# Performance work log

Measured on AMD Instinct MI355X. Metric: run time of the kernel, lower is better.

The kernel has to match this reference:

```python
import jax, jax.numpy as jnp
import numpy as np

D_MODEL = 1024
N_HEADS = 16
D_HEAD = D_MODEL // N_HEADS
D_FF = 4096
THETA = 10000.0
EPS = 1e-5


def rmsnorm(x, g):
    xf = x.astype(jnp.float32)
    rms = jnp.sqrt(jnp.mean(xf * xf, axis=-1, keepdims=True) + EPS)
    return ((xf / rms) * g).astype(x.dtype)


def rope(x, pos):
    # x: (B, H, S, d_head); pos: (S,) int
    dk = x.shape[-1]
    inv_freq = 1.0 / (THETA ** (jnp.arange(0, dk, 2, dtype=jnp.float32) / dk))
    freqs = pos.astype(jnp.float32)[:, None] * inv_freq[None, :]  # (S, dk/2)
    cos, sin = jnp.cos(freqs), jnp.sin(freqs)
    xp = x.reshape(*x.shape[:-1], dk // 2, 2)
    xe, xo = xp[..., 0], xp[..., 1]
    re = xe * cos - xo * sin
    ro = xe * sin + xo * cos
    return jnp.stack([re, ro], axis=-1).reshape(x.shape)


def attention(x, pos, q_w, k_w, v_w, o_w):
    B, S, D = x.shape
    def heads(t):
        return t.reshape(B, S, N_HEADS, D_HEAD).transpose(0, 2, 1, 3)
    Q = heads(x @ q_w.T)
    K = heads(x @ k_w.T)
    V = heads(x @ v_w.T)
    Q = rope(Q, pos)
    K = rope(K, pos)
    scores = jnp.einsum('bhqd,bhkd->bhqk', Q, K) / jnp.sqrt(jnp.float32(D_HEAD))
    causal = jnp.tril(jnp.ones((S, S), dtype=bool))
    scores = jnp.where(causal[None, None], scores, -jnp.inf)
    attn = jax.nn.softmax(scores, axis=-1)
    H = jnp.einsum('bhqk,bhkd->bhqd', attn, V)
    H = H.transpose(0, 2, 1, 3).reshape(B, S, D)
    return H @ o_w.T


def swiglu(x, w1, w2, w3):
    a = x @ w1.T
    swish = a * jax.nn.sigmoid(a)
    gate = x @ w3.T
    return (swish * gate) @ w2.T


def setup_inputs() -> dict:
    key = jax.random.key(0)
    ks = jax.random.split(key, 8)
    B, S = 4, 2048
    std_ff = (2.0 / (D_MODEL + D_FF)) ** 0.5
    return {
        'x': jax.random.normal(ks[0], (B, S, D_MODEL), jnp.float32),
        'token_positions': jnp.arange(S, dtype=jnp.int32),
        'q_w': jax.random.truncated_normal(ks[1], -3, 3, (D_MODEL, D_MODEL), jnp.float32),
        'k_w': jax.random.truncated_normal(ks[2], -3, 3, (D_MODEL, D_MODEL), jnp.float32),
        'v_w': jax.random.truncated_normal(ks[3], -3, 3, (D_MODEL, D_MODEL), jnp.float32),
        'o_w': jax.random.truncated_normal(ks[4], -3, 3, (D_MODEL, D_MODEL), jnp.float32),
        'g1': jnp.ones((D_MODEL,), jnp.float32),
        'g2': jnp.ones((D_MODEL,), jnp.float32),
        'w1': jax.random.truncated_normal(ks[5], -3, 3, (D_FF, D_MODEL), jnp.float32) * std_ff,
        'w2': jax.random.truncated_normal(ks[6], -3, 3, (D_MODEL, D_FF), jnp.float32) * std_ff,
        'w3': jax.random.truncated_normal(ks[7], -3, 3, (D_FF, D_MODEL), jnp.float32) * std_ff,
    }


def reference(x, token_positions, q_w, k_w, v_w, o_w, g1, g2, w1, w2, w3):
    x_norm = rmsnorm(x, g1)
    O = x + attention(x_norm, token_positions, q_w, k_w, v_w, o_w)
    H = O + swiglu(rmsnorm(O, g2), w1, w2, w3)
    return H
```

## Files before the change

### kernel.cpp

```cpp
#include <hip/hip_runtime.h>
#include <stdint.h>


typedef short bf16x8 __attribute__((ext_vector_type(8)));
typedef float f32x4  __attribute__((ext_vector_type(4)));

#define DEV static __device__ __forceinline__

DEV float bf2f(uint32_t u) { uint32_t v = u << 16; float f; __builtin_memcpy(&f, &v, 4); return f; }
DEV uint16_t f2bf(float f) {
  uint32_t u; __builtin_memcpy(&u, &f, 4);
  u = (u + 0x7fffu + ((u >> 16) & 1u)) >> 16;
  return (uint16_t)u;
}

DEV void gl_lds16(const uint16_t* g, uint16_t* l) {
  __builtin_amdgcn_global_load_lds((const __attribute__((address_space(1))) uint32_t*)g,
                                   (__attribute__((address_space(3))) uint32_t*)l, 16, 0, 0);
}


__global__ __launch_bounds__(256) void cvt_bf16_k(const float* __restrict__ src,
                                                  uint16_t* __restrict__ dst, int n4) {
  const int t = blockIdx.x * 256 + threadIdx.x;
  if (t >= n4) return;
  const float4 v = ((const float4*)src)[t];
  ushort4 o; o.x = f2bf(v.x); o.y = f2bf(v.y); o.z = f2bf(v.z); o.w = f2bf(v.w);
  ((ushort4*)dst)[t] = o;
}

__global__ __launch_bounds__(256) void cvt_split_qk_k(const float* __restrict__ qw,
                                                      const float* __restrict__ kw,
                                                      uint16_t* __restrict__ hi,
                                                      uint16_t* __restrict__ lo) {
  const int t = blockIdx.x * 256 + threadIdx.x;
  const int row = t >> 8, c4 = t & 255;
  const float* src = (row < 1024) ? (qw + (size_t)row * 1024)
                                  : (kw + (size_t)(row - 1024) * 1024);
  const float4 v = ((const float4*)src)[c4];
  ushort4 h, l;
  h.x = f2bf(v.x); l.x = f2bf(v.x - bf2f(h.x));
  h.y = f2bf(v.y); l.y = f2bf(v.y - bf2f(h.y));
  h.z = f2bf(v.z); l.z = f2bf(v.z - bf2f(h.z));
  h.w = f2bf(v.w); l.w = f2bf(v.w - bf2f(h.w));
  ((ushort4*)hi)[t] = h; ((ushort4*)lo)[t] = l;
}


template <bool SPLIT>
__global__ __launch_bounds__(256) void rmsnorm_k(const float* __restrict__ xin,
                                                 const float* __restrict__ g,
                                                 uint16_t* __restrict__ hi,
                                                 uint16_t* __restrict__ lo) {
  const int row = blockIdx.x, t = threadIdx.x;
  const float4 v = ((const float4*)(xin + (size_t)row * 1024))[t];
  float ss = v.x * v.x + v.y * v.y + v.z * v.z + v.w * v.w;
#pragma unroll
  for (int m = 1; m < 64; m <<= 1) ss += __shfl_xor(ss, m);
  __shared__ float red[4];
  if ((t & 63) == 0) red[t >> 6] = ss;
  __syncthreads();
  const float rinv = rsqrtf((red[0] + red[1] + red[2] + red[3]) * (1.0f / 1024.0f) + 1e-5f);
  const float4 gv = ((const float4*)g)[t];
  float y[4] = { v.x * rinv * gv.x, v.y * rinv * gv.y, v.z * rinv * gv.z, v.w * rinv * gv.w };
  ushort4 h; h.x = f2bf(y[0]); h.y = f2bf(y[1]); h.z = f2bf(y[2]); h.w = f2bf(y[3]);
  ((ushort4*)(hi + (size_t)row * 1024))[t] = h;
  if constexpr (SPLIT) {
    ushort4 l;
    l.x = f2bf(y[0] - bf2f(h.x)); l.y = f2bf(y[1] - bf2f(h.y));
    l.z = f2bf(y[2] - bf2f(h.z)); l.w = f2bf(y[3] - bf2f(h.w));
    ((ushort4*)(lo + (size_t)row * 1024))[t] = l;
  }
}


template <int OUT>
__global__ __launch_bounds__(256) void gemm_bt_k(const uint16_t* __restrict__ A,
                                                 const uint16_t* __restrict__ B,
                                                 void* __restrict__ C,
                                                 const float* __restrict__ resid,
                                                 int N, int K) {
  __shared__ __align__(16) uint16_t As[128 * 64];
  __shared__ __align__(16) uint16_t Bs[128 * 64];
  const int t = threadIdx.x, w = t >> 6, lane = t & 63, m16 = lane & 15, quad = lane >> 4;
  const int wm = (w >> 1) * 64, wn = (w & 1) * 64;
  const int mBase = blockIdx.y * 128, nBase = blockIdx.x * 128;
  f32x4 acc[4][4];
  const f32x4 vz = {0.f, 0.f, 0.f, 0.f};
#pragma unroll
  for (int i = 0; i < 4; ++i)
#pragma unroll
    for (int j = 0; j < 4; ++j) acc[i][j] = vz;
  const int r_ = t >> 3, g_ = t & 7, sg = g_ ^ (r_ & 7);
  const uint16_t* ag = A + (size_t)(mBase + r_) * K + sg * 8;
  const uint16_t* bg = B + (size_t)(nBase + r_) * K + sg * 8;
  for (int k0 = 0; k0 < K; k0 += 64) {
#pragma unroll
    for (int it = 0; it < 4; ++it) {
      gl_lds16(ag + (size_t)(it * 32) * K + k0, As + it * 2048 + t * 8);
      gl_lds16(bg + (size_t)(it * 32) * K + k0, Bs + it * 2048 + t * 8);
    }
    __syncthreads();
#pragma unroll
    for (int ks = 0; ks < 2; ++ks) {
      bf16x8 af[4], bf4[4];
      const int cg = ks * 4 + quad;
#pragma unroll
      for (int i = 0; i < 4; ++i) {
        const int rA = wm + i * 16 + m16;
        af[i] = *(const bf16x8*)(As + rA * 64 + ((cg ^ (rA & 7)) * 8));
        const int rB = wn + i * 16 + m16;
        bf4[i] = *(const bf16x8*)(Bs + rB * 64 + ((cg ^ (rB & 7)) * 8));
      }
#pragma unroll
      for (int i = 0; i < 4; ++i)
#pragma unroll
        for (int j = 0; j < 4; ++j)
          acc[i][j] = __builtin_amdgcn_mfma_f32_16x16x32_bf16(af[i], bf4[j], acc[i][j], 0, 0, 0);
    }
    __syncthreads();
  }
#pragma unroll
  for (int i = 0; i < 4; ++i) {
    const int row0 = mBase + wm + i * 16 + quad * 4;
#pragma unroll
    for (int j = 0; j < 4; ++j) {
      const int col = nBase + wn + j * 16 + m16;
#pragma unroll
      for (int r = 0; r < 4; ++r) {
        const size_t idx = (size_t)(row0 + r) * N + col;
        const float v = acc[i][j][r];
        if constexpr (OUT == 1) ((float*)C)[idx] = v + resid[idx];
        else                    ((uint16_t*)C)[idx] = f2bf(v);
      }
    }
  }
}


template <int OUT>
__global__ __launch_bounds__(512, 2) void gemm256_k(const uint16_t* __restrict__ A,
                                                    const uint16_t* __restrict__ B,
                                                    uint16_t* __restrict__ C,
                                                    const uint16_t* __restrict__ aux,
                                                    int N, int K) {
  __shared__ __align__(16) uint16_t As[2][256 * 64];
  __shared__ __align__(16) uint16_t Bs[2][256 * 64];
  const int t = threadIdx.x, w = t >> 6, lane = t & 63, m16 = lane & 15, quad = lane >> 4;
  const int wm = (w >> 2) * 128, wn = (w & 3) * 64;
  const int mBase = blockIdx.y * 256, nBase = blockIdx.x * 256;
  const int NT = K >> 6;

  f32x4 acc[8][4];
  const f32x4 vz = {0.f, 0.f, 0.f, 0.f};
#pragma unroll
  for (int i = 0; i < 8; ++i)
#pragma unroll
    for (int j = 0; j < 4; ++j) acc[i][j] = vz;

  const int r_ = t >> 3, g_ = t & 7, sg = g_ ^ (r_ & 7);
  const uint16_t* ag = A + (size_t)(mBase + r_) * K + sg * 8;
  const uint16_t* bg = B + (size_t)(nBase + r_) * K + sg * 8;

#define STG_A(kt, h)                                                         \
  if ((kt) < NT) {                                                           \
    uint16_t* d0 = &As[(kt) & 1][(h) * 8192 + t * 8];                        \
    const uint16_t* s0 = ag + (size_t)((h) * 128) * K + (kt) * 64;           \
    gl_lds16(s0, d0);                                                        \
    gl_lds16(s0 + (size_t)64 * K, d0 + 4096);                                \
  }
#define STG_B(kt, h)                                                         \
  if ((kt) < NT) {                                                           \
    uint16_t* d0 = &Bs[(kt) & 1][(h) * 8192 + t * 8];                        \
    const uint16_t* s0 = bg + (size_t)((h) * 128) * K + (kt) * 64;           \
    gl_lds16(s0, d0);                                                        \
    gl_lds16(s0 + (size_t)64 * K, d0 + 4096);                                \
  }

  STG_B(0, 0); STG_B(0, 1); STG_A(0, 0); STG_A(0, 1);
  STG_B(1, 0); STG_A(1, 0);

  for (int T = 0; T < NT; ++T) {
    const int c = T & 1;
    const uint16_t* Ac = As[c];
    const uint16_t* Bc = Bs[c];
    bf16x8 af[4][2], b0[2][2], b1[2][2];

    STG_B(T + 1, 1);
    if (T == NT - 1) { asm volatile("s_waitcnt vmcnt(0)" ::: "memory"); }
    else             { asm volatile("s_waitcnt vmcnt(6)" ::: "memory"); }
    __builtin_amdgcn_s_barrier();
    __builtin_amdgcn_sched_barrier(0);
#pragma unroll
    for (int i = 0; i < 4; ++i) {
      const int rA = wm + i * 16 + m16;
#pragma unroll
      for (int ks = 0; ks < 2; ++ks)
        af[i][ks] = *(const bf16x8*)(Ac + rA * 64 + (((ks * 4 + quad) ^ (rA & 7)) * 8));
    }
#pragma unroll
    for (int j = 0; j < 2; ++j) {
      const int rB = wn + j * 16 + m16;
#pragma unroll
      for (int ks = 0; ks < 2; ++ks)
        b0[j][ks] = *(const bf16x8*)(Bc + rB * 64 + (((ks * 4 + quad) ^ (rB & 7)) * 8));
    }
    __builtin_amdgcn_s_setprio(1);
#pragma unroll
    for (int ks = 0; ks < 2; ++ks)
#pragma unroll
      for (int i = 0; i < 4; ++i)
#pragma unroll
        for (int j = 0; j < 2; ++j)
          acc[i][j] = __builtin_amdgcn_mfma_f32_16x16x32_bf16(af[i][ks], b0[j][ks], acc[i][j], 0, 0, 0);
    __builtin_amdgcn_s_setprio(0);
    __builtin_amdgcn_s_barrier();

    STG_A(T + 1, 1);
#pragma unroll
    for (int j = 0; j < 2; ++j) {
      const int rB = wn + (2 + j) * 16 + m16;
#pragma unroll
      for (int ks = 0; ks < 2; ++ks)
        b1[j][ks] = *(const bf16x8*)(Bc + rB * 64 + (((ks * 4 + quad) ^ (rB & 7)) * 8));
    }
    __builtin_amdgcn_s_setprio(1);
#pragma unroll
    for (int ks = 0; ks < 2; ++ks)
#pragma unroll
      for (int i = 0; i < 4; ++i)
#pragma unroll
        for (int j = 0; j < 2; ++j)
          acc[i][2 + j] = __builtin_amdgcn_mfma_f32_16x16x32_bf16(af[i][ks], b1[j][ks], acc[i][2 + j], 0, 0, 0);
    __builtin_amdgcn_s_setprio(0);
    __builtin_amdgcn_s_barrier();

    STG_B(T + 2, 0);
#pragma unroll
    for (int i = 0; i < 4; ++i) {
      const int rA = wm + 64 + i * 16 + m16;
#pragma unroll
      for (int ks = 0; ks < 2; ++ks)
        af[i][ks] = *(const bf16x8*)(Ac + rA * 64 + (((ks * 4 + quad) ^ (rA & 7)) * 8));
    }
    __builtin_amdgcn_s_setprio(1);
#pragma unroll
    for (int ks = 0; ks < 2; ++ks)
#pragma unroll
      for (int i = 0; i < 4; ++i)
#pragma unroll
        for (int j = 0; j < 2; ++j)
          acc[4 + i][j] = __builtin_amdgcn_mfma_f32_16x16x32_bf16(af[i][ks], b0[j][ks], acc[4 + i][j], 0, 0, 0);
    __builtin_amdgcn_s_setprio(0);
    __builtin_amdgcn_s_barrier();

    STG_A(T + 2, 0);
    __builtin_amdgcn_s_setprio(1);
#pragma unroll
    for (int ks = 0; ks < 2; ++ks)
#pragma unroll
      for (int i = 0; i < 4; ++i)
#pragma unroll
        for (int j = 0; j < 2; ++j)
          acc[4 + i][2 + j] = __builtin_amdgcn_mfma_f32_16x16x32_bf16(af[i][ks], b1[j][ks], acc[4 + i][2 + j], 0, 0, 0);
    __builtin_amdgcn_s_setprio(0);
    __builtin_amdgcn_s_barrier();
  }
#undef STG_A
#undef STG_B

#pragma unroll
  for (int i = 0; i < 8; ++i) {
    const int row0 = mBase + wm + i * 16 + quad * 4;
#pragma unroll
    for (int j = 0; j < 4; ++j) {
      const int col = nBase + wn + j * 16 + m16;
#pragma unroll
      for (int r = 0; r < 4; ++r) {
        const size_t idx = (size_t)(row0 + r) * N + col;
        const float v = acc[i][j][r];
        if constexpr (OUT == 2) {
          const float a = bf2f(aux[idx]);
          const float sw = a / (1.f + __expf(-a));
          C[idx] = f2bf(sw * v);
        } else {
          C[idx] = f2bf(v);
        }
      }
    }
  }
}


__global__ __launch_bounds__(512, 2) void gemm_split256_k(
    const uint16_t* __restrict__ Ahi, const uint16_t* __restrict__ Alo,
    const uint16_t* __restrict__ Bhi, const uint16_t* __restrict__ Blo,
    uint16_t* __restrict__ Chi, uint16_t* __restrict__ Clo, int N, int K) {
  __shared__ __align__(16) uint16_t Ah[2][256 * 32];
  __shared__ __align__(16) uint16_t Al[2][256 * 32];
  __shared__ __align__(16) uint16_t Bh[2][256 * 32];
  __shared__ __align__(16) uint16_t Bl[2][256 * 32];
  const int t = threadIdx.x, w = t >> 6, lane = t & 63, m16 = lane & 15, quad = lane >> 4;
  const int wm = (w >> 2) * 128, wn = (w & 3) * 64;
  const int mBase = blockIdx.y * 256, nBase = blockIdx.x * 256;
  const int NT = K >> 5;

  f32x4 acc[8][4];
  const f32x4 vz = {0.f, 0.f, 0.f, 0.f};
#pragma unroll
  for (int i = 0; i < 8; ++i)
#pragma unroll
    for (int j = 0; j < 4; ++j) acc[i][j] = vz;

  const int r_ = t >> 2, g_ = t & 3, sg = g_ ^ (r_ & 3);
  const uint16_t* agh = Ahi + (size_t)(mBase + r_) * K + sg * 8;
  const uint16_t* agl = Alo + (size_t)(mBase + r_) * K + sg * 8;
  const uint16_t* bgh = Bhi + (size_t)(nBase + r_) * K + sg * 8;
  const uint16_t* bgl = Blo + (size_t)(nBase + r_) * K + sg * 8;

#define STG4(OP, base, kt)                                                   \
  if ((kt) < NT) {                                                           \
    uint16_t* d = &OP[(kt) & 1][t * 8];                                      \
    const uint16_t* s = (base) + (size_t)(kt) * 32;                          \
    gl_lds16(s, d);                                                          \
    gl_lds16(s + (size_t)128 * K, d + 4096);                                 \
  }

  STG4(Bh, bgh, 0); STG4(Bl, bgl, 0);
  STG4(Ah, agh, 0); STG4(Al, agl, 0);
  STG4(Bh, bgh, 1); STG4(Bl, bgl, 1);

  for (int T = 0; T < NT; ++T) {
    const int c = T & 1;
    bf16x8 a_h[4], a_l[4], b0h[2], b0l[2], b1h[2], b1l[2];

    STG4(Ah, agh, T + 1);
    if (T == NT - 1) { asm volatile("s_waitcnt vmcnt(0)" ::: "memory"); }
    else             { asm volatile("s_waitcnt vmcnt(6)" ::: "memory"); }
    __builtin_amdgcn_s_barrier();
    __builtin_amdgcn_sched_barrier(0);
#pragma unroll
    for (int i = 0; i < 4; ++i) {
      const int rA = wm + i * 16 + m16;
      const int offA = rA * 32 + ((quad ^ (rA & 3)) * 8);
      a_h[i] = *(const bf16x8*)(&Ah[c][offA]);
      a_l[i] = *(const bf16x8*)(&Al[c][offA]);
    }
#pragma unroll
    for (int j = 0; j < 2; ++j) {
      const int rB = wn + j * 16 + m16;
      const int offB = rB * 32 + ((quad ^ (rB & 3)) * 8);
      b0h[j] = *(const bf16x8*)(&Bh[c][offB]);
      b0l[j] = *(const bf16x8*)(&Bl[c][offB]);
    }
    __builtin_amdgcn_s_setprio(1);
#pragma unroll
    for (int i = 0; i < 4; ++i)
#pragma unroll
      for (int j = 0; j < 2; ++j) {
        acc[i][j] = __builtin_amdgcn_mfma_f32_16x16x32_bf16(a_h[i], b0h[j], acc[i][j], 0, 0, 0);
        acc[i][j] = __builtin_amdgcn_mfma_f32_16x16x32_bf16(a_h[i], b0l[j], acc[i][j], 0, 0, 0);
        acc[i][j] = __builtin_amdgcn_mfma_f32_16x16x32_bf16(a_l[i], b0h[j], acc[i][j], 0, 0, 0);
      }
    __builtin_amdgcn_s_setprio(0);
    __builtin_amdgcn_s_barrier();

    STG4(Al, agl, T + 1);
#pragma unroll
    for (int j = 0; j < 2; ++j) {
      const int rB = wn + (2 + j) * 16 + m16;
      const int offB = rB * 32 + ((quad ^ (rB & 3)) * 8);
      b1h[j] = *(const bf16x8*)(&Bh[c][offB]);
      b1l[j] = *(const bf16x8*)(&Bl[c][offB]);
    }
    __builtin_amdgcn_s_setprio(1);
#pragma unroll
    for (int i = 0; i < 4; ++i)
#pragma unroll
      for (int j = 0; j < 2; ++j) {
        acc[i][2 + j] = __builtin_amdgcn_mfma_f32_16x16x32_bf16(a_h[i], b1h[j], acc[i][2 + j], 0, 0, 0);
        acc[i][2 + j] = __builtin_amdgcn_mfma_f32_16x16x32_bf16(a_h[i], b1l[j], acc[i][2 + j], 0, 0, 0);
        acc[i][2 + j] = __builtin_amdgcn_mfma_f32_16x16x32_bf16(a_l[i], b1h[j], acc[i][2 + j], 0, 0, 0);
      }
    __builtin_amdgcn_s_setprio(0);
    __builtin_amdgcn_s_barrier();

    STG4(Bh, bgh, T + 2);
#pragma unroll
    for (int i = 0; i < 4; ++i) {
      const int rA = wm + 64 + i * 16 + m16;
      const int offA = rA * 32 + ((quad ^ (rA & 3)) * 8);
      a_h[i] = *(const bf16x8*)(&Ah[c][offA]);
      a_l[i] = *(const bf16x8*)(&Al[c][offA]);
    }
    __builtin_amdgcn_s_setprio(1);
#pragma unroll
    for (int i = 0; i < 4; ++i)
#pragma unroll
      for (int j = 0; j < 2; ++j) {
        acc[4 + i][j] = __builtin_amdgcn_mfma_f32_16x16x32_bf16(a_h[i], b0h[j], acc[4 + i][j], 0, 0, 0);
        acc[4 + i][j] = __builtin_amdgcn_mfma_f32_16x16x32_bf16(a_h[i], b0l[j], acc[4 + i][j], 0, 0, 0);
        acc[4 + i][j] = __builtin_amdgcn_mfma_f32_16x16x32_bf16(a_l[i], b0h[j], acc[4 + i][j], 0, 0, 0);
      }
    __builtin_amdgcn_s_setprio(0);
    __builtin_amdgcn_s_barrier();

    STG4(Bl, bgl, T + 2);
    __builtin_amdgcn_s_setprio(1);
#pragma unroll
    for (int i = 0; i < 4; ++i)
#pragma unroll
      for (int j = 0; j < 2; ++j) {
        acc[4 + i][2 + j] = __builtin_amdgcn_mfma_f32_16x16x32_bf16(a_h[i], b1h[j], acc[4 + i][2 + j], 0, 0, 0);
        acc[4 + i][2 + j] = __builtin_amdgcn_mfma_f32_16x16x32_bf16(a_h[i], b1l[j], acc[4 + i][2 + j], 0, 0, 0);
        acc[4 + i][2 + j] = __builtin_amdgcn_mfma_f32_16x16x32_bf16(a_l[i], b1h[j], acc[4 + i][2 + j], 0, 0, 0);
      }
    __builtin_amdgcn_s_setprio(0);
    __builtin_amdgcn_s_barrier();
  }
#undef STG4

#pragma unroll
  for (int i = 0; i < 8; ++i) {
    const int row0 = mBase + wm + i * 16 + quad * 4;
#pragma unroll
    for (int j = 0; j < 4; ++j) {
      const int col = nBase + wn + j * 16 + m16;
#pragma unroll
      for (int r = 0; r < 4; ++r) {
        const size_t idx = (size_t)(row0 + r) * N + col;
        const float v = acc[i][j][r];
        const uint16_t hh = f2bf(v);
        Chi[idx] = hh;
        Clo[idx] = f2bf(v - bf2f(hh));
      }
    }
  }
}


__global__ __launch_bounds__(256) void rope_k(uint16_t* __restrict__ qkh,
                                              uint16_t* __restrict__ qkl,
                                              const int* __restrict__ pos) {
  const int u = blockIdx.x * 256 + threadIdx.x;
  const int row = u >> 8, p = (u & 255) * 4;
  const int which = p >> 9, hp = p & 511, h = hp >> 5, d2 = hp & 31;
  const size_t idx = (size_t)row * 2048 + which * 1024 + h * 64 + d2 * 2;
  union { uint4 v; uint32_t w[4]; } vh, vl, oh, ol;
  vh.v = *(const uint4*)(qkh + idx);
  vl.v = *(const uint4*)(qkl + idx);
  const float fp = (float)pos[row & 2047];
#pragma unroll
  for (int e = 0; e < 4; ++e) {
    const float xe = bf2f(vh.w[e] & 0xffffu) + bf2f(vl.w[e] & 0xffffu);
    const float xo = bf2f(vh.w[e] >> 16) + bf2f(vl.w[e] >> 16);
    const float inv_freq = exp2f((float)(d2 + e) * -0.41524101186092029f);
    const float fr = fp * inv_freq;
    float sn, cs; sincosf(fr, &sn, &cs);
    const float re = xe * cs - xo * sn;
    const float ro = xe * sn + xo * cs;
    const uint16_t reh = f2bf(re), roh = f2bf(ro);
    const uint16_t rel = f2bf(re - bf2f(reh)), rol = f2bf(ro - bf2f(roh));
    oh.w[e] = (uint32_t)reh | ((uint32_t)roh << 16);
    ol.w[e] = (uint32_t)rel | ((uint32_t)rol << 16);
  }
  *(uint4*)(qkh + idx) = oh.v;
  *(uint4*)(qkl + idx) = ol.v;
}


__global__ __launch_bounds__(256) void flash_k(const uint16_t* __restrict__ Qh,
                                               const uint16_t* __restrict__ Ql,
                                               const uint16_t* __restrict__ Vt,
                                               uint16_t* __restrict__ Hout) {
  __shared__ __align__(16) uint16_t Kh[2][64 * 64];
  __shared__ __align__(16) uint16_t Kl[2][64 * 64];
  __shared__ __align__(16) uint16_t Vs[2][64 * 64];
  __shared__ __align__(16) uint16_t P[4][32 * 72];

  const int bh = blockIdx.y, b = bh >> 4, h = bh & 15;
  const int t = threadIdx.x, w = t >> 6, lane = t & 63, m16 = lane & 15, quad = lane >> 4;

  const int r_ = t >> 3, g_ = t & 7, sgx = g_ ^ (r_ & 7);
  const uint16_t* khg = Qh + (size_t)(b * 2048 + r_) * 2048 + 1024 + h * 64 + sgx * 8;
  const uint16_t* klg = Ql + (size_t)(b * 2048 + r_) * 2048 + 1024 + h * 64 + sgx * 8;
  const uint16_t* vtg = Vt + (size_t)(h * 64 + r_) * 8192 + (size_t)b * 2048 + sgx * 8;

  const float nscl = 0.18033688011112042f;

  for (int half = 0; half < 2; ++half) {
    const int qt = half ? (15 - (int)blockIdx.x) : (int)blockIdx.x;

    bf16x8 qh[2][2], ql[2][2];
#pragma unroll
    for (int i = 0; i < 2; ++i) {
      const int row = b * 2048 + qt * 128 + w * 32 + i * 16 + m16;
#pragma unroll
      for (int ks = 0; ks < 2; ++ks) {
        const size_t offq = (size_t)row * 2048 + h * 64 + ks * 32 + quad * 8;
        qh[i][ks] = *(const bf16x8*)(Qh + offq);
        ql[i][ks] = *(const bf16x8*)(Ql + offq);
      }
    }
#pragma unroll
    for (int i = 0; i < 2; ++i)
#pragma unroll
      for (int ks = 0; ks < 2; ++ks)
        asm volatile("" : "+v"(qh[i][ks]), "+v"(ql[i][ks]));

    const int ktEnd = 2 * qt + 2;

#pragma unroll
    for (int it = 0; it < 2; ++it) {
      gl_lds16(khg + (size_t)(it * 32) * 2048, &Kh[0][it * 2048 + t * 8]);
      gl_lds16(klg + (size_t)(it * 32) * 2048, &Kl[0][it * 2048 + t * 8]);
      gl_lds16(vtg + (size_t)(it * 32) * 8192, &Vs[0][it * 2048 + t * 8]);
    }

    float mr[2][4], lr[2][4];
    f32x4 o[2][4];
    const f32x4 vz = {0.f, 0.f, 0.f, 0.f};
#pragma unroll
    for (int i = 0; i < 2; ++i)
#pragma unroll
      for (int r = 0; r < 4; ++r) { mr[i][r] = -1e30f; lr[i][r] = 0.f; }
#pragma unroll
    for (int i = 0; i < 2; ++i)
#pragma unroll
      for (int n = 0; n < 4; ++n) o[i][n] = vz;

    for (int kt = 0; kt < ktEnd; ++kt) {
      const int cur = kt & 1, nxt = cur ^ 1;
      __builtin_amdgcn_s_barrier();
      __builtin_amdgcn_sched_barrier(0);
      if (kt + 1 < ktEnd) {
        const int kn = kt + 1;
#pragma unroll
        for (int it = 0; it < 2; ++it) {
          gl_lds16(khg + (size_t)(kn * 64 + it * 32) * 2048, &Kh[nxt][it * 2048 + t * 8]);
          gl_lds16(klg + (size_t)(kn * 64 + it * 32) * 2048, &Kl[nxt][it * 2048 + t * 8]);
          gl_lds16(vtg + (size_t)(it * 32) * 8192 + kn * 64, &Vs[nxt][it * 2048 + t * 8]);
        }
        asm volatile("s_waitcnt vmcnt(6)" ::: "memory");
      } else {
        asm volatile("s_waitcnt vmcnt(0)" ::: "memory");
      }
      __builtin_amdgcn_s_barrier();
      __builtin_amdgcn_sched_barrier(0);

      f32x4 sc[2][4];
#pragma unroll
      for (int i = 0; i < 2; ++i)
#pragma unroll
        for (int j = 0; j < 4; ++j) sc[i][j] = vz;
#pragma unroll
      for (int ks = 0; ks < 2; ++ks) {
        bf16x8 kfh[4], kfl[4];
        const int cg = ks * 4 + quad;
#pragma unroll
        for (int j = 0; j < 4; ++j) {
          const int rK = j * 16 + m16;
          const int offk = rK * 64 + ((cg ^ (rK & 7)) * 8);
          kfh[j] = *(const bf16x8*)(&Kh[cur][offk]);
          kfl[j] = *(const bf16x8*)(&Kl[cur][offk]);
        }
        __builtin_amdgcn_s_setprio(1);
#pragma unroll
        for (int i = 0; i < 2; ++i)
#pragma unroll
          for (int j = 0; j < 4; ++j) {
            sc[i][j] = __builtin_amdgcn_mfma_f32_16x16x32_bf16(qh[i][ks], kfh[j], sc[i][j], 0, 0, 0);
            sc[i][j] = __builtin_amdgcn_mfma_f32_16x16x32_bf16(qh[i][ks], kfl[j], sc[i][j], 0, 0, 0);
            sc[i][j] = __builtin_amdgcn_mfma_f32_16x16x32_bf16(ql[i][ks], kfh[j], sc[i][j], 0, 0, 0);
          }
        __builtin_amdgcn_s_setprio(0);
      }

#pragma unroll
      for (int i = 0; i < 2; ++i) {
        const bool needMask = (kt * 64 + 63) > (qt * 128 + w * 32 + i * 16);
#pragma unroll
        for (int r = 0; r < 4; ++r) {
          float mx = -1e30f;
          if (needMask) {
            const int qg = qt * 128 + w * 32 + i * 16 + quad * 4 + r;
#pragma unroll
            for (int j = 0; j < 4; ++j) {
              float v = sc[i][j][r];
              const int kg = kt * 64 + j * 16 + m16;
              if (kg > qg) v = -1e30f;
              sc[i][j][r] = v;
              mx = fmaxf(mx, v);
            }
          } else {
#pragma unroll
            for (int j = 0; j < 4; ++j) mx = fmaxf(mx, sc[i][j][r]);
          }
#pragma unroll
          for (int m = 1; m < 16; m <<= 1) mx = fmaxf(mx, __shfl_xor(mx, m));
          const float mnew = fmaxf(mr[i][r], mx);
          const float alpha = __builtin_amdgcn_exp2f((mr[i][r] - mnew) * nscl);
          mr[i][r] = mnew;
          const float nm = mnew * nscl;
          float ls = 0.f;
#pragma unroll
          for (int j = 0; j < 4; ++j) {
            const float pv = __builtin_amdgcn_exp2f(__builtin_fmaf(sc[i][j][r], nscl, -nm));
            sc[i][j][r] = pv;
            ls += pv;
          }
#pragma unroll
          for (int m = 1; m < 16; m <<= 1) ls += __shfl_xor(ls, m);
          lr[i][r] = lr[i][r] * alpha + ls;
#pragma unroll
          for (int n = 0; n < 4; ++n) o[i][n][r] *= alpha;
        }
#pragma unroll
        for (int j = 0; j < 4; ++j)
#pragma unroll
          for (int r = 0; r < 4; ++r)
            P[w][(i * 16 + quad * 4 + r) * 72 + j * 16 + m16] = f2bf(sc[i][j][r]);
      }

#pragma unroll
      for (int ks2 = 0; ks2 < 2; ++ks2) {
        bf16x8 pf[2], vf[4];
#pragma unroll
        for (int i = 0; i < 2; ++i)
          pf[i] = *(const bf16x8*)(&P[w][(i * 16 + m16) * 72 + ks2 * 32 + quad * 8]);
        const int cg = ks2 * 4 + quad;
#pragma unroll
        for (int n = 0; n < 4; ++n) {
          const int rV = n * 16 + m16;
          vf[n] = *(const bf16x8*)(&Vs[cur][rV * 64 + ((cg ^ (rV & 7)) * 8)]);
        }
        __builtin_amdgcn_s_setprio(1);
#pragma unroll
        for (int i = 0; i < 2; ++i)
#pragma unroll
          for (int n = 0; n < 4; ++n)
            o[i][n] = __builtin_amdgcn_mfma_f32_16x16x32_bf16(pf[i], vf[n], o[i][n], 0, 0, 0);
        __builtin_amdgcn_s_setprio(0);
      }
    }

#pragma unroll
    for (int i = 0; i < 2; ++i)
#pragma unroll
      for (int r = 0; r < 4; ++r) {
        const float inv = 1.f / lr[i][r];
        const size_t row = (size_t)(b * 2048 + qt * 128 + w * 32 + i * 16 + quad * 4 + r);
#pragma unroll
        for (int n = 0; n < 4; ++n)
          Hout[row * 1024 + h * 64 + n * 16 + m16] = f2bf(o[i][n][r] * inv);
      }
    __syncthreads();
  }
}


extern "C" void kernel_launch(void* const* d_in, const int* in_sizes, int n_in,
                              void* d_out, int out_size, void* d_ws, size_t ws_size,
                              hipStream_t stream) {
  (void)in_sizes; (void)n_in; (void)out_size; (void)ws_size;
  const float* x   = (const float*)d_in[0];
  const int*   pos = (const int*)  d_in[1];
  const float* q_w = (const float*)d_in[2];
  const float* k_w = (const float*)d_in[3];
  const float* v_w = (const float*)d_in[4];
  const float* o_w = (const float*)d_in[5];
  const float* g1  = (const float*)d_in[6];
  const float* g2  = (const float*)d_in[7];
  const float* w1  = (const float*)d_in[8];
  const float* w2  = (const float*)d_in[9];
  const float* w3  = (const float*)d_in[10];

  char* ws = (char*)d_ws;
  uint16_t* wqk_hi = (uint16_t*)(ws + 0);
  uint16_t* wqk_lo = (uint16_t*)(ws + 4194304);
  uint16_t* wv     = (uint16_t*)(ws + 8388608);
  uint16_t* wo     = (uint16_t*)(ws + 10485760);
  uint16_t* w1b    = (uint16_t*)(ws + 12582912);
  uint16_t* w3b    = (uint16_t*)(ws + 20971520);
  uint16_t* w2b    = (uint16_t*)(ws + 29360128);
  uint16_t* xn_hi  = (uint16_t*)(ws + 37748736);
  uint16_t* xn_lo  = (uint16_t*)(ws + 54525952);
  uint16_t* vt     = (uint16_t*)(ws + 88080384);
  uint16_t* qk_hi  = (uint16_t*)(ws + 104857600);
  uint16_t* qk_lo  = (uint16_t*)(ws + 138412032);
  uint16_t* hbuf   = (uint16_t*)(ws + 171966464);
  float*    ores   = (float*)   (ws + 188743680);
  uint16_t* on2    = (uint16_t*)(ws + 222298112);
  uint16_t* abuf   = (uint16_t*)(ws + 104857600);
  uint16_t* gbuf   = (uint16_t*)(ws + 37748736);

  cvt_split_qk_k<<<2048, 256, 0, stream>>>(q_w, k_w, wqk_hi, wqk_lo);
  cvt_bf16_k<<<1024, 256, 0, stream>>>(v_w, wv, 262144);
  cvt_bf16_k<<<1024, 256, 0, stream>>>(o_w, wo, 262144);
  cvt_bf16_k<<<4096, 256, 0, stream>>>(w1, w1b, 1048576);
  cvt_bf16_k<<<4096, 256, 0, stream>>>(w3, w3b, 1048576);
  cvt_bf16_k<<<4096, 256, 0, stream>>>(w2, w2b, 1048576);

  rmsnorm_k<true><<<8192, 256, 0, stream>>>(x, g1, xn_hi, xn_lo);

  gemm_split256_k<<<dim3(8, 32), 512, 0, stream>>>(xn_hi, xn_lo, wqk_hi, wqk_lo,
                                                   qk_hi, qk_lo, 2048, 1024);
  gemm_bt_k<0><<<dim3(64, 8), 256, 0, stream>>>(wv, xn_hi, (void*)vt, nullptr, 8192, 1024);

  rope_k<<<8192, 256, 0, stream>>>(qk_hi, qk_lo, pos);

  flash_k<<<dim3(8, 64), 256, 0, stream>>>(qk_hi, qk_lo, vt, hbuf);

  gemm_bt_k<1><<<dim3(8, 64), 256, 0, stream>>>(hbuf, wo, (void*)ores, x, 1024, 1024);

  rmsnorm_k<false><<<8192, 256, 0, stream>>>(ores, g2, on2, nullptr);

  gemm256_k<0><<<dim3(16, 32), 512, 0, stream>>>(on2, w1b, abuf, nullptr, 4096, 1024);
  gemm256_k<2><<<dim3(16, 32), 512, 0, stream>>>(on2, w3b, gbuf, abuf, 4096, 1024);

  gemm_bt_k<1><<<dim3(8, 64), 256, 0, stream>>>(gbuf, w2b, d_out, ores, 1024, 4096);
}
```

Before: 851.5 us.

## Fuse RoPE into QK split GEMM epilogue and pack bf16 conversion in flash

Applies rotary embedding directly in the epilogue of the split-precision QK GEMM, using a lane shuffle to pair even and odd columns, and removes the separate rope kernel. This drops one launch and a full read-modify-write pass over the hi/lo QK buffers. The flash kernel also converts P to bf16 with the packed v_cvt_pk_bf16_f32 instruction instead of software rounding. In exchange the GEMM epilogue now does per-element sincos work, and the hardware conversion's rounding may differ slightly from the manual f2bf.

```diff
diff --git a/kernel.cpp b/kernel.cpp
--- a/kernel.cpp
+++ b/kernel.cpp
@@ -295,7 +295,8 @@
 __global__ __launch_bounds__(512, 2) void gemm_split256_k(
     const uint16_t* __restrict__ Ahi, const uint16_t* __restrict__ Alo,
     const uint16_t* __restrict__ Bhi, const uint16_t* __restrict__ Blo,
-    uint16_t* __restrict__ Chi, uint16_t* __restrict__ Clo, int N, int K) {
+    uint16_t* __restrict__ Chi, uint16_t* __restrict__ Clo,
+    const int* __restrict__ pos, int N, int K) {
   __shared__ __align__(16) uint16_t Ah[2][256 * 32];
   __shared__ __align__(16) uint16_t Al[2][256 * 32];
   __shared__ __align__(16) uint16_t Bh[2][256 * 32];
@@ -420,52 +421,36 @@
   }
 #undef STG4
 
+  float invf[4];
+#pragma unroll
+  for (int j = 0; j < 4; ++j) {
+    const int col = nBase + wn + j * 16 + m16;
+    invf[j] = exp2f((float)((col & 63) >> 1) * -0.41524101186092029f);
+  }
+  const bool oddc = (m16 & 1) != 0;
 #pragma unroll
   for (int i = 0; i < 8; ++i) {
     const int row0 = mBase + wm + i * 16 + quad * 4;
 #pragma unroll
-    for (int j = 0; j < 4; ++j) {
-      const int col = nBase + wn + j * 16 + m16;
-#pragma unroll
-      for (int r = 0; r < 4; ++r) {
-        const size_t idx = (size_t)(row0 + r) * N + col;
+    for (int r = 0; r < 4; ++r) {
+      const int row = row0 + r;
+      const float fp = (float)pos[row & 2047];
+      const size_t rb = (size_t)row * N;
+#pragma unroll
+      for (int j = 0; j < 4; ++j) {
         const float v = acc[i][j][r];
-        const uint16_t hh = f2bf(v);
+        const float pv = __shfl_xor(v, 1);
+        const float xe = oddc ? pv : v;
+        const float xo = oddc ? v : pv;
+        float sn, cs; sincosf(fp * invf[j], &sn, &cs);
+        const float vr = oddc ? (xe * sn + xo * cs) : (xe * cs - xo * sn);
+        const size_t idx = rb + (nBase + wn + j * 16 + m16);
+        const uint16_t hh = f2bf(vr);
         Chi[idx] = hh;
-        Clo[idx] = f2bf(v - bf2f(hh));
-      }
-    }
-  }
-}
-
-
-__global__ __launch_bounds__(256) void rope_k(uint16_t* __restrict__ qkh,
-                                              uint16_t* __restrict__ qkl,
-                                              const int* __restrict__ pos) {
-  const int u = blockIdx.x * 256 + threadIdx.x;
-  const int row = u >> 8, p = (u & 255) * 4;
-  const int which = p >> 9, hp = p & 511, h = hp >> 5, d2 = hp & 31;
-  const size_t idx = (size_t)row * 2048 + which * 1024 + h * 64 + d2 * 2;
-  union { uint4 v; uint32_t w[4]; } vh, vl, oh, ol;
-  vh.v = *(const uint4*)(qkh + idx);
-  vl.v = *(const uint4*)(qkl + idx);
-  const float fp = (float)pos[row & 2047];
-#pragma unroll
-  for (int e = 0; e < 4; ++e) {
-    const float xe = bf2f(vh.w[e] & 0xffffu) + bf2f(vl.w[e] & 0xffffu);
-    const float xo = bf2f(vh.w[e] >> 16) + bf2f(vl.w[e] >> 16);
-    const float inv_freq = exp2f((float)(d2 + e) * -0.41524101186092029f);
-    const float fr = fp * inv_freq;
-    float sn, cs; sincosf(fr, &sn, &cs);
-    const float re = xe * cs - xo * sn;
-    const float ro = xe * sn + xo * cs;
-    const uint16_t reh = f2bf(re), roh = f2bf(ro);
-    const uint16_t rel = f2bf(re - bf2f(reh)), rol = f2bf(ro - bf2f(roh));
-    oh.w[e] = (uint32_t)reh | ((uint32_t)roh << 16);
-    ol.w[e] = (uint32_t)rel | ((uint32_t)rol << 16);
-  }
-  *(uint4*)(qkh + idx) = oh.v;
-  *(uint4*)(qkl + idx) = ol.v;
+        Clo[idx] = f2bf(vr - bf2f(hh));
+      }
+    }
+  }
 }
 
 
@@ -616,10 +601,18 @@
           for (int n = 0; n < 4; ++n) o[i][n][r] *= alpha;
         }
 #pragma unroll
-        for (int j = 0; j < 4; ++j)
-#pragma unroll
-          for (int r = 0; r < 4; ++r)
-            P[w][(i * 16 + quad * 4 + r) * 72 + j * 16 + m16] = f2bf(sc[i][j][r]);
+        for (int j = 0; j < 4; ++j) {
+          uint32_t pk01, pk23;
+          asm("v_cvt_pk_bf16_f32 %0, %1, %2"
+              : "=v"(pk01) : "v"(sc[i][j][0]), "v"(sc[i][j][1]));
+          asm("v_cvt_pk_bf16_f32 %0, %1, %2"
+              : "=v"(pk23) : "v"(sc[i][j][2]), "v"(sc[i][j][3]));
+          const int pb = (i * 16 + quad * 4) * 72 + j * 16 + m16;
+          P[w][pb]       = (uint16_t)pk01;
+          P[w][pb + 72]  = (uint16_t)(pk01 >> 16);
+          P[w][pb + 144] = (uint16_t)pk23;
+          P[w][pb + 216] = (uint16_t)(pk23 >> 16);
+        }
       }
 
 #pragma unroll
@@ -704,10 +697,8 @@
   rmsnorm_k<true><<<8192, 256, 0, stream>>>(x, g1, xn_hi, xn_lo);
 
   gemm_split256_k<<<dim3(8, 32), 512, 0, stream>>>(xn_hi, xn_lo, wqk_hi, wqk_lo,
-                                                   qk_hi, qk_lo, 2048, 1024);
+                                                   qk_hi, qk_lo, pos, 2048, 1024);
   gemm_bt_k<0><<<dim3(64, 8), 256, 0, stream>>>(wv, xn_hi, (void*)vt, nullptr, 8192, 1024);
-
-  rope_k<<<8192, 256, 0, stream>>>(qk_hi, qk_lo, pos);
 
   flash_k<<<dim3(8, 64), 256, 0, stream>>>(qk_hi, qk_lo, vt, hbuf);
 
```

Measured after the change: 840.4 us. No clear change (-1.3%).
